# Kernel tuning notes

Hardware: AMD Instinct MI355X
Metric: run time of the kernel (lower is better)

Reference implementation:

```python
import jax, jax.numpy as jnp
import numpy as np

N_NODES = 100000
N_RELS = 4
N_EDGES = 200000
D_IN = 256
D_OUT = 256
N_BASES = 2
LN_EPS = 1e-5


def setup_inputs() -> dict:
    key = jax.random.key(0)
    ks = jax.random.split(key, 8)
    x = jax.random.normal(ks[0], (N_NODES, D_IN), dtype=jnp.float32)
    src_idx = jax.random.randint(ks[1], (N_RELS, N_EDGES), 0, N_NODES, dtype=jnp.int32)
    dst_idx = jax.random.randint(ks[2], (N_RELS, N_EDGES), 0, N_NODES, dtype=jnp.int32)
    # WeightBasis: bases [B, in, out], per-relation coefficients [R, B]
    xav = float(np.sqrt(2.0)) * float(np.sqrt(6.0 / (D_IN + D_OUT)))
    bases = jax.random.uniform(ks[3], (N_BASES, D_IN, D_OUT), minval=-xav, maxval=xav, dtype=jnp.float32)
    w_comp = jax.random.normal(ks[4], (N_RELS, N_BASES), dtype=jnp.float32) * 0.5
    loop_weight = jax.random.uniform(ks[5], (D_IN, D_OUT), minval=-xav, maxval=xav, dtype=jnp.float32)
    h_bias = jnp.zeros((D_OUT,), dtype=jnp.float32)
    ln_gamma = jnp.ones((D_OUT,), dtype=jnp.float32)
    ln_beta = jnp.zeros((D_OUT,), dtype=jnp.float32)
    return {"x": x, "src_idx": src_idx, "dst_idx": dst_idx, "bases": bases,
            "w_comp": w_comp, "loop_weight": loop_weight, "h_bias": h_bias,
            "ln_gamma": ln_gamma, "ln_beta": ln_beta}


def reference(x, src_idx, dst_idx, bases, w_comp, loop_weight, h_bias, ln_gamma, ln_beta):
    n = x.shape[0]
    # basis combination -> per-relation weights [R, in, out]
    W = jnp.einsum('rb,bio->rio', w_comp, bases)

    def per_rel(W_r, s, d):
        # GraphConv(norm='right', weight=W_r): aggregate src feats to dst,
        # normalize by in-degree (clamped to 1), then matmul.
        msgs = x[s]                                            # [E, in]
        agg = jax.ops.segment_sum(msgs, d, num_segments=n)     # [N, in]
        deg = jax.ops.segment_sum(jnp.ones(d.shape, x.dtype), d, num_segments=n)
        agg = agg / jnp.maximum(deg, 1.0)[:, None]
        return agg @ W_r                                        # [N, out]

    hs = jax.vmap(per_rel)(W, src_idx, dst_idx).sum(axis=0)    # HeteroGraphConv sum aggregate
    # self-loop + bias
    h = hs + x @ loop_weight + h_bias
    # layer norm
    mu = jnp.mean(h, axis=-1, keepdims=True)
    var = jnp.mean(jnp.square(h - mu), axis=-1, keepdims=True)
    h = (h - mu) * jax.lax.rsqrt(var + LN_EPS) * ln_gamma + ln_beta
    # activation (dropout inactive in eval; NGNN has 0 layers)
    return jax.nn.relu(h)
```

## Files before the change

### kernel.cpp

```cpp
#include <hip/hip_runtime.h>


#define NN 100000
#define NR 4
#define NE 200000
#define KDIM 768
#define CAP 64

typedef __attribute__((ext_vector_type(8))) short short8;
typedef __attribute__((ext_vector_type(16))) float floatx16;

__device__ __forceinline__ unsigned short f2bf(float f) {
  unsigned u = __float_as_uint(f);
  u += 0x7FFFu + ((u >> 16) & 1u);
  return (unsigned short)(u >> 16);
}

__device__ __forceinline__ void gload16(const unsigned short* g, unsigned short* l) {
  __builtin_amdgcn_global_load_lds(
      (const __attribute__((address_space(1))) unsigned int*)g,
      (__attribute__((address_space(3))) unsigned int*)l, 16, 0, 0);
}

__global__ void build_edges(const int* __restrict__ src, const int* __restrict__ dst,
                            int* __restrict__ cnt, int* __restrict__ edgebuf) {
  int i = blockIdx.x * 256 + threadIdx.x;
  if (i >= NR * NE) return;
  int r = i / NE;
  int s = src[i];
  int d = dst[i];
  int pos = atomicAdd(&cnt[d], 1);
  if (pos < CAP) edgebuf[d * CAP + pos] = s | (r << 20);
}

__global__ void build_bt(const float* __restrict__ bases, const float* __restrict__ loop_w,
                         unsigned short* __restrict__ Bt) {
  int i = blockIdx.x * 256 + threadIdx.x;
  int n = i & 255;
  int k = i >> 8;
  float v;
  if (k < 256)      v = bases[k * 256 + n];
  else if (k < 512) v = bases[65536 + (k - 256) * 256 + n];
  else              v = loop_w[(k - 512) * 256 + n];
  Bt[(size_t)n * KDIM + k] = f2bf(v);
}

__global__ void conv_x(const float* __restrict__ x, unsigned short* __restrict__ A) {
  int q = blockIdx.x * 256 + threadIdx.x;
  int row = q >> 6;
  int c4 = (q & 63) << 2;
  const float4 v = *(const float4*)(x + (size_t)row * 256 + c4);
  ushort4 u;
  u.x = f2bf(v.x); u.y = f2bf(v.y); u.z = f2bf(v.z); u.w = f2bf(v.w);
  *(ushort4*)(A + (size_t)row * KDIM + 512 + c4) = u;
}

__global__ void agg_edges(const int* __restrict__ edgebuf, const int* __restrict__ cnt,
                          const float* __restrict__ w_comp, unsigned short* __restrict__ A) {
  const int wave = threadIdx.x >> 6;
  const int lane = threadIdx.x & 63;
  const int d = blockIdx.x * 4 + wave;

  int c = cnt[d]; c = c < CAP ? c : CAP;
  int ev = 0;
  if (lane < c) ev = edgebuf[d * CAP + lane];
  const int rl = ev >> 20;

  float s00, s01, s02, s03, s10, s11, s12, s13;
  {
    float d0 = (float)__popcll(__ballot(lane < c && rl == 0));
    float d1 = (float)__popcll(__ballot(lane < c && rl == 1));
    float d2 = (float)__popcll(__ballot(lane < c && rl == 2));
    float d3 = (float)__popcll(__ballot(lane < c && rl == 3));
    float i0 = 1.0f / fmaxf(d0, 1.0f), i1 = 1.0f / fmaxf(d1, 1.0f);
    float i2 = 1.0f / fmaxf(d2, 1.0f), i3 = 1.0f / fmaxf(d3, 1.0f);
    s00 = w_comp[0] * i0; s10 = w_comp[1] * i0;
    s01 = w_comp[2] * i1; s11 = w_comp[3] * i1;
    s02 = w_comp[4] * i2; s12 = w_comp[5] * i2;
    s03 = w_comp[6] * i3; s13 = w_comp[7] * i3;
  }

  float a0[4] = {0.f, 0.f, 0.f, 0.f};
  float a1[4] = {0.f, 0.f, 0.f, 0.f};
  const unsigned short* Xl = A + 512 + lane * 4;

#define EDGE_W(v, w0, w1)                                            \
  int r_##w0 = (v) >> 20;                                            \
  float w0 = r_##w0 < 2 ? (r_##w0 == 0 ? s00 : s01)                  \
                        : (r_##w0 == 2 ? s02 : s03);                 \
  float w1 = r_##w0 < 2 ? (r_##w0 == 0 ? s10 : s11)                  \
                        : (r_##w0 == 2 ? s12 : s13);

#define ACCUM(g, w0, w1)                                             \
  {                                                                  \
    float e0 = __uint_as_float((g).x << 16);                         \
    float e1 = __uint_as_float((g).x & 0xFFFF0000u);                 \
    float e2 = __uint_as_float((g).y << 16);                         \
    float e3 = __uint_as_float((g).y & 0xFFFF0000u);                 \
    a0[0] += (w0) * e0; a0[1] += (w0) * e1;                          \
    a0[2] += (w0) * e2; a0[3] += (w0) * e3;                          \
    a1[0] += (w1) * e0; a1[1] += (w1) * e1;                          \
    a1[2] += (w1) * e2; a1[3] += (w1) * e3;                          \
  }

  int i = 0;
  for (; i + 4 <= c; i += 4) {
    int v0 = __shfl(ev, i);
    int v1 = __shfl(ev, i + 1);
    int v2 = __shfl(ev, i + 2);
    int v3 = __shfl(ev, i + 3);
    const uint2 g0 = *(const uint2*)(Xl + (size_t)(v0 & 0xFFFFF) * KDIM);
    const uint2 g1 = *(const uint2*)(Xl + (size_t)(v1 & 0xFFFFF) * KDIM);
    const uint2 g2 = *(const uint2*)(Xl + (size_t)(v2 & 0xFFFFF) * KDIM);
    const uint2 g3 = *(const uint2*)(Xl + (size_t)(v3 & 0xFFFFF) * KDIM);
    { EDGE_W(v0, w0a, w1a) ACCUM(g0, w0a, w1a) }
    { EDGE_W(v1, w0b, w1b) ACCUM(g1, w0b, w1b) }
    { EDGE_W(v2, w0c, w1c) ACCUM(g2, w0c, w1c) }
    { EDGE_W(v3, w0d, w1d) ACCUM(g3, w0d, w1d) }
  }
  for (; i < c; ++i) {
    int v = __shfl(ev, i);
    const uint2 g = *(const uint2*)(Xl + (size_t)(v & 0xFFFFF) * KDIM);
    EDGE_W(v, w0, w1)
    ACCUM(g, w0, w1)
  }

  ushort4 u0, u1;
  u0.x = f2bf(a0[0]); u0.y = f2bf(a0[1]); u0.z = f2bf(a0[2]); u0.w = f2bf(a0[3]);
  u1.x = f2bf(a1[0]); u1.y = f2bf(a1[1]); u1.z = f2bf(a1[2]); u1.w = f2bf(a1[3]);
  *(ushort4*)(A + (size_t)d * KDIM + lane * 4) = u0;
  *(ushort4*)(A + (size_t)d * KDIM + 256 + lane * 4) = u1;
}

#define BM 128
__launch_bounds__(256, 2)
__global__ void gemm_ln(const unsigned short* __restrict__ A, const unsigned short* __restrict__ Bt,
                        const float* __restrict__ h_bias, const float* __restrict__ gamma,
                        const float* __restrict__ beta, float* __restrict__ out) {
  __shared__ unsigned short As[BM * 32];
  __shared__ unsigned short Bs[256 * 32];
  const int tid = threadIdx.x;
  const int wave = tid >> 6;
  const int lane = tid & 63;
  const int l31 = lane & 31;
  const int half = lane >> 5;
  const int m0 = blockIdx.x * BM;

  floatx16 acc[8];
#pragma unroll
  for (int t = 0; t < 8; ++t)
#pragma unroll
    for (int r = 0; r < 16; ++r) acc[t][r] = 0.0f;

  const int prow = 16 * wave + (lane >> 2);
  const int lc = (lane & 3) ^ ((prow >> 1) & 3);
  const unsigned short* gA = A + (size_t)(m0 + prow) * KDIM + lc * 8;
  const unsigned short* gB = Bt + (size_t)prow * KDIM + lc * 8;
  unsigned short* lA = As + 16 * wave * 32 + lane * 8;
  unsigned short* lB = Bs + 16 * wave * 32 + lane * 8;

  const int sw = (l31 >> 1) & 3;
  const int rA32 = (wave * 32 + l31) * 32;

  for (int k0 = 0; k0 < KDIM; k0 += 32) {
    gload16(gA, lA);
    gload16(gA + 64 * KDIM, lA + 64 * 32);
    gload16(gB, lB);
    gload16(gB + 64 * KDIM, lB + 64 * 32);
    gload16(gB + 128 * KDIM, lB + 128 * 32);
    gload16(gB + 192 * KDIM, lB + 192 * 32);
    gA += 32;
    gB += 32;
    __syncthreads();
#pragma unroll
    for (int kk = 0; kk < 2; ++kk) {
      const int pc = ((kk * 2 + half) ^ sw) * 8;
      short8 af = *(const short8*)(&As[rA32 + pc]);
#pragma unroll
      for (int t = 0; t < 8; ++t) {
        short8 bfr = *(const short8*)(&Bs[(t * 32 + l31) * 32 + pc]);
        acc[t] = __builtin_amdgcn_mfma_f32_32x32x16_bf16(af, bfr, acc[t], 0, 0, 0);
      }
    }
    __syncthreads();
  }

  float bcol[8], gc[8], bc[8];
#pragma unroll
  for (int t = 0; t < 8; ++t) {
    int col = t * 32 + l31;
    bcol[t] = h_bias[col];
    gc[t] = gamma[col];
    bc[t] = beta[col];
  }
#pragma unroll
  for (int t = 0; t < 8; ++t)
#pragma unroll
    for (int r = 0; r < 16; ++r) acc[t][r] += bcol[t];

  const int m_base = m0 + wave * 32;
#pragma unroll
  for (int r = 0; r < 16; ++r) {
    float s = 0.f, q = 0.f;
#pragma unroll
    for (int t = 0; t < 8; ++t) { float v = acc[t][r]; s += v; q += v * v; }
#pragma unroll
    for (int m = 16; m >= 1; m >>= 1) {
      s += __shfl_xor(s, m);
      q += __shfl_xor(q, m);
    }
    float mean = s * (1.0f / 256.0f);
    float var = q * (1.0f / 256.0f) - mean * mean;
    float rstd = rsqrtf(var + 1e-5f);
    int row = (r & 3) + ((r >> 2) << 3) + (half << 2);
    int grow = m_base + row;
    if (grow < NN) {
#pragma unroll
      for (int t = 0; t < 8; ++t) {
        float v = (acc[t][r] - mean) * rstd * gc[t] + bc[t];
        out[(size_t)grow * 256 + t * 32 + l31] = fmaxf(v, 0.0f);
      }
    }
  }
}

extern "C" void kernel_launch(void* const* d_in, const int* in_sizes, int n_in,
                              void* d_out, int out_size, void* d_ws, size_t ws_size,
                              hipStream_t stream) {
  const float* x      = (const float*)d_in[0];
  const int*   src    = (const int*)d_in[1];
  const int*   dst    = (const int*)d_in[2];
  const float* bases  = (const float*)d_in[3];
  const float* w_comp = (const float*)d_in[4];
  const float* loop_w = (const float*)d_in[5];
  const float* h_bias = (const float*)d_in[6];
  const float* gamma  = (const float*)d_in[7];
  const float* beta   = (const float*)d_in[8];
  float* out = (float*)d_out;

  char* ws = (char*)d_ws;
  unsigned short* A  = (unsigned short*)ws;
  unsigned short* Bt = (unsigned short*)(ws + 153600000);
  int* cnt     = (int*)(ws + 153993216);
  int* edgebuf = (int*)(ws + 154393216);

  hipMemsetAsync(cnt, 0, 400000, stream);

  build_edges<<<(NR * NE + 255) / 256, 256, 0, stream>>>(src, dst, cnt, edgebuf);
  build_bt<<<768, 256, 0, stream>>>(bases, loop_w, Bt);
  conv_x<<<25000, 256, 0, stream>>>(x, A);
  agg_edges<<<25000, 256, 0, stream>>>(edgebuf, cnt, w_comp, A);
  gemm_ln<<<(NN + BM - 1) / BM, 256, 0, stream>>>(A, Bt, h_bias, gamma, beta, out);
}
```

Baseline: 403.7 us.

## Fuse prep kernels, widen edge gathers, and restructure GEMM LDS tile layout

The x conversion, weight transpose and edge-bucketing kernels are merged into one launch, which cuts launch overhead and lets their work overlap. agg_edges now handles two destination nodes per wave with half-waves, each lane gathering 16-byte rows of 8 features, with the per-node edge capacity lowered to 32. The GEMM stages A and B in LDS in an MFMA-fragment-ordered layout instead of a swizzled row layout, so fragment reads need no XOR indexing. Lowering the capacity could silently drop edges for nodes with very high in-degree.

```diff
diff --git a/kernel.cpp b/kernel.cpp
--- a/kernel.cpp
+++ b/kernel.cpp
@@ -5,7 +5,8 @@
 #define NR 4
 #define NE 200000
 #define KDIM 768
-#define CAP 64
+#define CAP 32
+#define BM 128
 
 typedef __attribute__((ext_vector_type(8))) short short8;
 typedef __attribute__((ext_vector_type(16))) float floatx16;
@@ -22,67 +23,72 @@
       (__attribute__((address_space(3))) unsigned int*)l, 16, 0, 0);
 }
 
-__global__ void build_edges(const int* __restrict__ src, const int* __restrict__ dst,
-                            int* __restrict__ cnt, int* __restrict__ edgebuf) {
-  int i = blockIdx.x * 256 + threadIdx.x;
-  if (i >= NR * NE) return;
-  int r = i / NE;
-  int s = src[i];
-  int d = dst[i];
-  int pos = atomicAdd(&cnt[d], 1);
-  if (pos < CAP) edgebuf[d * CAP + pos] = s | (r << 20);
-}
-
-__global__ void build_bt(const float* __restrict__ bases, const float* __restrict__ loop_w,
-                         unsigned short* __restrict__ Bt) {
-  int i = blockIdx.x * 256 + threadIdx.x;
-  int n = i & 255;
-  int k = i >> 8;
-  float v;
-  if (k < 256)      v = bases[k * 256 + n];
-  else if (k < 512) v = bases[65536 + (k - 256) * 256 + n];
-  else              v = loop_w[(k - 512) * 256 + n];
-  Bt[(size_t)n * KDIM + k] = f2bf(v);
-}
-
-__global__ void conv_x(const float* __restrict__ x, unsigned short* __restrict__ A) {
-  int q = blockIdx.x * 256 + threadIdx.x;
-  int row = q >> 6;
-  int c4 = (q & 63) << 2;
-  const float4 v = *(const float4*)(x + (size_t)row * 256 + c4);
-  ushort4 u;
-  u.x = f2bf(v.x); u.y = f2bf(v.y); u.z = f2bf(v.z); u.w = f2bf(v.w);
-  *(ushort4*)(A + (size_t)row * KDIM + 512 + c4) = u;
+__global__ void prep(const float* __restrict__ x, const float* __restrict__ bases,
+                     const float* __restrict__ loop_w, const int* __restrict__ src,
+                     const int* __restrict__ dst, unsigned short* __restrict__ A,
+                     unsigned short* __restrict__ Bt, int* __restrict__ cnt,
+                     int* __restrict__ edgebuf) {
+  const int b = blockIdx.x;
+  const int tid = threadIdx.x;
+  if (b < 25000) {
+    int q = b * 256 + tid;
+    int row = q >> 6;
+    int c4 = (q & 63) << 2;
+    const float4 v = *(const float4*)(x + (size_t)row * 256 + c4);
+    ushort4 u;
+    u.x = f2bf(v.x); u.y = f2bf(v.y); u.z = f2bf(v.z); u.w = f2bf(v.w);
+    *(ushort4*)(A + (size_t)row * KDIM + 512 + c4) = u;
+  } else if (b < 25768) {
+    int i = (b - 25000) * 256 + tid;
+    int n = i & 255;
+    int k = i >> 8;
+    float v;
+    if (k < 256)      v = bases[k * 256 + n];
+    else if (k < 512) v = bases[65536 + (k - 256) * 256 + n];
+    else              v = loop_w[(k - 512) * 256 + n];
+    Bt[(size_t)n * KDIM + k] = f2bf(v);
+  } else {
+    int i = (b - 25768) * 256 + tid;
+    int r = i / NE;
+    int s = src[i];
+    int dd = dst[i];
+    int pos = atomicAdd(&cnt[dd], 1);
+    if (pos < CAP) edgebuf[dd * CAP + pos] = s | (r << 20);
+  }
 }
 
 __global__ void agg_edges(const int* __restrict__ edgebuf, const int* __restrict__ cnt,
                           const float* __restrict__ w_comp, unsigned short* __restrict__ A) {
-  const int wave = threadIdx.x >> 6;
-  const int lane = threadIdx.x & 63;
-  const int d = blockIdx.x * 4 + wave;
-
-  int c = cnt[d]; c = c < CAP ? c : CAP;
+  const int tid = threadIdx.x;
+  const int lane = tid & 63;
+  const int wave = tid >> 6;
+  const int half = lane >> 5;
+  const int l31 = lane & 31;
+  const int d = blockIdx.x * 8 + wave * 2 + half;
+
+  int cc = cnt[d]; cc = cc < CAP ? cc : CAP;
   int ev = 0;
-  if (lane < c) ev = edgebuf[d * CAP + lane];
+  if (l31 < cc) ev = edgebuf[d * CAP + l31];
   const int rl = ev >> 20;
 
-  float s00, s01, s02, s03, s10, s11, s12, s13;
-  {
-    float d0 = (float)__popcll(__ballot(lane < c && rl == 0));
-    float d1 = (float)__popcll(__ballot(lane < c && rl == 1));
-    float d2 = (float)__popcll(__ballot(lane < c && rl == 2));
-    float d3 = (float)__popcll(__ballot(lane < c && rl == 3));
-    float i0 = 1.0f / fmaxf(d0, 1.0f), i1 = 1.0f / fmaxf(d1, 1.0f);
-    float i2 = 1.0f / fmaxf(d2, 1.0f), i3 = 1.0f / fmaxf(d3, 1.0f);
-    s00 = w_comp[0] * i0; s10 = w_comp[1] * i0;
-    s01 = w_comp[2] * i1; s11 = w_comp[3] * i1;
-    s02 = w_comp[4] * i2; s12 = w_comp[5] * i2;
-    s03 = w_comp[6] * i3; s13 = w_comp[7] * i3;
-  }
-
-  float a0[4] = {0.f, 0.f, 0.f, 0.f};
-  float a1[4] = {0.f, 0.f, 0.f, 0.f};
-  const unsigned short* Xl = A + 512 + lane * 4;
+  unsigned long long b0 = __ballot((l31 < cc) && rl == 0);
+  unsigned long long b1 = __ballot((l31 < cc) && rl == 1);
+  unsigned long long b2 = __ballot((l31 < cc) && rl == 2);
+  unsigned long long b3 = __ballot((l31 < cc) && rl == 3);
+  const int sh = half << 5;
+  float i0 = 1.0f / fmaxf((float)__popc((unsigned)(b0 >> sh)), 1.0f);
+  float i1 = 1.0f / fmaxf((float)__popc((unsigned)(b1 >> sh)), 1.0f);
+  float i2 = 1.0f / fmaxf((float)__popc((unsigned)(b2 >> sh)), 1.0f);
+  float i3 = 1.0f / fmaxf((float)__popc((unsigned)(b3 >> sh)), 1.0f);
+  float s00 = w_comp[0] * i0, s10 = w_comp[1] * i0;
+  float s01 = w_comp[2] * i1, s11 = w_comp[3] * i1;
+  float s02 = w_comp[4] * i2, s12 = w_comp[5] * i2;
+  float s03 = w_comp[6] * i3, s13 = w_comp[7] * i3;
+
+  float a0[8] = {0.f, 0.f, 0.f, 0.f, 0.f, 0.f, 0.f, 0.f};
+  float a1[8] = {0.f, 0.f, 0.f, 0.f, 0.f, 0.f, 0.f, 0.f};
+  const unsigned short* Xp = A + 512 + l31 * 8;
+  const int selbase = lane & 32;
 
 #define EDGE_W(v, w0, w1)                                            \
   int r_##w0 = (v) >> 20;                                            \
@@ -91,54 +97,65 @@
   float w1 = r_##w0 < 2 ? (r_##w0 == 0 ? s10 : s11)                  \
                         : (r_##w0 == 2 ? s12 : s13);
 
-#define ACCUM(g, w0, w1)                                             \
+#define ACC8(g, w0, w1)                                              \
   {                                                                  \
     float e0 = __uint_as_float((g).x << 16);                         \
     float e1 = __uint_as_float((g).x & 0xFFFF0000u);                 \
     float e2 = __uint_as_float((g).y << 16);                         \
     float e3 = __uint_as_float((g).y & 0xFFFF0000u);                 \
-    a0[0] += (w0) * e0; a0[1] += (w0) * e1;                          \
-    a0[2] += (w0) * e2; a0[3] += (w0) * e3;                          \
-    a1[0] += (w1) * e0; a1[1] += (w1) * e1;                          \
-    a1[2] += (w1) * e2; a1[3] += (w1) * e3;                          \
+    float e4 = __uint_as_float((g).z << 16);                         \
+    float e5 = __uint_as_float((g).z & 0xFFFF0000u);                 \
+    float e6 = __uint_as_float((g).w << 16);                         \
+    float e7 = __uint_as_float((g).w & 0xFFFF0000u);                 \
+    a0[0] += (w0) * e0; a0[1] += (w0) * e1; a0[2] += (w0) * e2;      \
+    a0[3] += (w0) * e3; a0[4] += (w0) * e4; a0[5] += (w0) * e5;      \
+    a0[6] += (w0) * e6; a0[7] += (w0) * e7;                          \
+    a1[0] += (w1) * e0; a1[1] += (w1) * e1; a1[2] += (w1) * e2;      \
+    a1[3] += (w1) * e3; a1[4] += (w1) * e4; a1[5] += (w1) * e5;      \
+    a1[6] += (w1) * e6; a1[7] += (w1) * e7;                          \
   }
 
   int i = 0;
-  for (; i + 4 <= c; i += 4) {
-    int v0 = __shfl(ev, i);
-    int v1 = __shfl(ev, i + 1);
-    int v2 = __shfl(ev, i + 2);
-    int v3 = __shfl(ev, i + 3);
-    const uint2 g0 = *(const uint2*)(Xl + (size_t)(v0 & 0xFFFFF) * KDIM);
-    const uint2 g1 = *(const uint2*)(Xl + (size_t)(v1 & 0xFFFFF) * KDIM);
-    const uint2 g2 = *(const uint2*)(Xl + (size_t)(v2 & 0xFFFFF) * KDIM);
-    const uint2 g3 = *(const uint2*)(Xl + (size_t)(v3 & 0xFFFFF) * KDIM);
-    { EDGE_W(v0, w0a, w1a) ACCUM(g0, w0a, w1a) }
-    { EDGE_W(v1, w0b, w1b) ACCUM(g1, w0b, w1b) }
-    { EDGE_W(v2, w0c, w1c) ACCUM(g2, w0c, w1c) }
-    { EDGE_W(v3, w0d, w1d) ACCUM(g3, w0d, w1d) }
-  }
-  for (; i < c; ++i) {
-    int v = __shfl(ev, i);
-    const uint2 g = *(const uint2*)(Xl + (size_t)(v & 0xFFFFF) * KDIM);
+  for (; i + 4 <= cc; i += 4) {
+    int v0 = __shfl(ev, selbase + i);
+    int v1 = __shfl(ev, selbase + i + 1);
+    int v2 = __shfl(ev, selbase + i + 2);
+    int v3 = __shfl(ev, selbase + i + 3);
+    const uint4 g0 = *(const uint4*)(Xp + (size_t)(v0 & 0xFFFFF) * KDIM);
+    const uint4 g1 = *(const uint4*)(Xp + (size_t)(v1 & 0xFFFFF) * KDIM);
+    const uint4 g2 = *(const uint4*)(Xp + (size_t)(v2 & 0xFFFFF) * KDIM);
+    const uint4 g3 = *(const uint4*)(Xp + (size_t)(v3 & 0xFFFFF) * KDIM);
+    { EDGE_W(v0, w0a, w1a) ACC8(g0, w0a, w1a) }
+    { EDGE_W(v1, w0b, w1b) ACC8(g1, w0b, w1b) }
+    { EDGE_W(v2, w0c, w1c) ACC8(g2, w0c, w1c) }
+    { EDGE_W(v3, w0d, w1d) ACC8(g3, w0d, w1d) }
+  }
+  for (; i < cc; ++i) {
+    int v = __shfl(ev, selbase + i);
+    const uint4 g = *(const uint4*)(Xp + (size_t)(v & 0xFFFFF) * KDIM);
     EDGE_W(v, w0, w1)
-    ACCUM(g, w0, w1)
-  }
-
-  ushort4 u0, u1;
-  u0.x = f2bf(a0[0]); u0.y = f2bf(a0[1]); u0.z = f2bf(a0[2]); u0.w = f2bf(a0[3]);
-  u1.x = f2bf(a1[0]); u1.y = f2bf(a1[1]); u1.z = f2bf(a1[2]); u1.w = f2bf(a1[3]);
-  *(ushort4*)(A + (size_t)d * KDIM + lane * 4) = u0;
-  *(ushort4*)(A + (size_t)d * KDIM + 256 + lane * 4) = u1;
-}
-
-#define BM 128
+    ACC8(g, w0, w1)
+  }
+
+  uint4 o0, o1;
+  o0.x = (unsigned)f2bf(a0[0]) | ((unsigned)f2bf(a0[1]) << 16);
+  o0.y = (unsigned)f2bf(a0[2]) | ((unsigned)f2bf(a0[3]) << 16);
+  o0.z = (unsigned)f2bf(a0[4]) | ((unsigned)f2bf(a0[5]) << 16);
+  o0.w = (unsigned)f2bf(a0[6]) | ((unsigned)f2bf(a0[7]) << 16);
+  o1.x = (unsigned)f2bf(a1[0]) | ((unsigned)f2bf(a1[1]) << 16);
+  o1.y = (unsigned)f2bf(a1[2]) | ((unsigned)f2bf(a1[3]) << 16);
+  o1.z = (unsigned)f2bf(a1[4]) | ((unsigned)f2bf(a1[5]) << 16);
+  o1.w = (unsigned)f2bf(a1[6]) | ((unsigned)f2bf(a1[7]) << 16);
+  *(uint4*)(A + (size_t)d * KDIM + l31 * 8) = o0;
+  *(uint4*)(A + (size_t)d * KDIM + 256 + l31 * 8) = o1;
+}
+
 __launch_bounds__(256, 2)
 __global__ void gemm_ln(const unsigned short* __restrict__ A, const unsigned short* __restrict__ Bt,
                         const float* __restrict__ h_bias, const float* __restrict__ gamma,
                         const float* __restrict__ beta, float* __restrict__ out) {
-  __shared__ unsigned short As[BM * 32];
-  __shared__ unsigned short Bs[256 * 32];
+  __shared__ unsigned short As[4 * 2 * 512];
+  __shared__ unsigned short Bs[8 * 2 * 512];
   const int tid = threadIdx.x;
   const int wave = tid >> 6;
   const int lane = tid & 63;
@@ -152,33 +169,32 @@
 #pragma unroll
     for (int r = 0; r < 16; ++r) acc[t][r] = 0.0f;
 
-  const int prow = 16 * wave + (lane >> 2);
-  const int lc = (lane & 3) ^ ((prow >> 1) & 3);
-  const unsigned short* gA = A + (size_t)(m0 + prow) * KDIM + lc * 8;
-  const unsigned short* gB = Bt + (size_t)prow * KDIM + lc * 8;
-  unsigned short* lA = As + 16 * wave * 32 + lane * 8;
-  unsigned short* lB = Bs + 16 * wave * 32 + lane * 8;
-
-  const int sw = (l31 >> 1) & 3;
-  const int rA32 = (wave * 32 + l31) * 32;
+  int arow = m0 + wave * 32 + l31;
+  if (arow >= NN) arow = NN - 1;
+  const unsigned short* gA = A + (size_t)arow * KDIM + half * 8;
+  const unsigned short* gBa = Bt + (size_t)(wave * 64 + l31) * KDIM + half * 8;
+  const unsigned short* gBb = gBa + 32 * KDIM;
+  unsigned short* lA0 = As + (wave * 2 + 0) * 512 + lane * 8;
+  unsigned short* lA1 = As + (wave * 2 + 1) * 512 + lane * 8;
+  unsigned short* lB0 = Bs + ((wave * 2 + 0) * 2 + 0) * 512 + lane * 8;
+  unsigned short* lB1 = Bs + ((wave * 2 + 0) * 2 + 1) * 512 + lane * 8;
+  unsigned short* lB2 = Bs + ((wave * 2 + 1) * 2 + 0) * 512 + lane * 8;
+  unsigned short* lB3 = Bs + ((wave * 2 + 1) * 2 + 1) * 512 + lane * 8;
 
   for (int k0 = 0; k0 < KDIM; k0 += 32) {
-    gload16(gA, lA);
-    gload16(gA + 64 * KDIM, lA + 64 * 32);
-    gload16(gB, lB);
-    gload16(gB + 64 * KDIM, lB + 64 * 32);
-    gload16(gB + 128 * KDIM, lB + 128 * 32);
-    gload16(gB + 192 * KDIM, lB + 192 * 32);
-    gA += 32;
-    gB += 32;
+    gload16(gA + k0, lA0);
+    gload16(gA + k0 + 16, lA1);
+    gload16(gBa + k0, lB0);
+    gload16(gBa + k0 + 16, lB1);
+    gload16(gBb + k0, lB2);
+    gload16(gBb + k0 + 16, lB3);
     __syncthreads();
 #pragma unroll
     for (int kk = 0; kk < 2; ++kk) {
-      const int pc = ((kk * 2 + half) ^ sw) * 8;
-      short8 af = *(const short8*)(&As[rA32 + pc]);
+      short8 af = *(const short8*)(As + (wave * 2 + kk) * 512 + lane * 8);
 #pragma unroll
       for (int t = 0; t < 8; ++t) {
-        short8 bfr = *(const short8*)(&Bs[(t * 32 + l31) * 32 + pc]);
+        short8 bfr = *(const short8*)(Bs + (t * 2 + kk) * 512 + lane * 8);
         acc[t] = __builtin_amdgcn_mfma_f32_32x32x16_bf16(af, bfr, acc[t], 0, 0, 0);
       }
     }
@@ -246,9 +262,7 @@
 
   hipMemsetAsync(cnt, 0, 400000, stream);
 
-  build_edges<<<(NR * NE + 255) / 256, 256, 0, stream>>>(src, dst, cnt, edgebuf);
-  build_bt<<<768, 256, 0, stream>>>(bases, loop_w, Bt);
-  conv_x<<<25000, 256, 0, stream>>>(x, A);
-  agg_edges<<<25000, 256, 0, stream>>>(edgebuf, cnt, w_comp, A);
+  prep<<<28893, 256, 0, stream>>>(x, bases, loop_w, src, dst, A, Bt, cnt, edgebuf);
+  agg_edges<<<12500, 256, 0, stream>>>(edgebuf, cnt, w_comp, A);
   gemm_ln<<<(NN + BM - 1) / BM, 256, 0, stream>>>(A, Bt, h_bias, gamma, beta, out);
 }
```

Result: slower. 413.4 us (+2.4%).
